# Kernel tuning notes

Hardware: AMD Instinct MI355X
Metric: run time of the kernel (lower is better)

The kernel has to match this reference:

```python
import jax, jax.numpy as jnp
import numpy as np

NUM_HEADS = 8
D_CONV = 4
NORMALIZER = 16.0
LN_EPS = 1e-5


def setup_inputs() -> dict:
    key = jax.random.key(0)
    ks = jax.random.split(key, 9)
    B, L, E = 4, 2048, 1024
    dk = E // 2
    return {
        "x": jax.random.normal(ks[0], (B, L, E), jnp.float32),
        "conv_w": jax.random.normal(ks[1], (E, D_CONV), jnp.float32) * 0.3,
        "wq": jax.random.normal(ks[2], (E, dk), jnp.float32) * 0.02,
        "wkg": jax.random.normal(ks[3], (E, dk), jnp.float32) * 0.02,
        "wv": jax.random.normal(ks[4], (E, E), jnp.float32) * 0.02,
        "wg": jax.random.normal(ks[5], (E, E), jnp.float32) * 0.02,
        "bg": jax.random.normal(ks[6], (E,), jnp.float32) * 0.02,
        "wout": jax.random.normal(ks[7], (E, E), jnp.float32) * 0.02,
        "aug_balance": jax.random.normal(ks[8], (dk,), jnp.float32) * 0.1,
    }


def _causal_dwconv_silu(x, w):
    # x: [B, L, E]; w: [E, W] depthwise kernel. Causal: left-pad W-1 zeros.
    xt = jnp.transpose(x, (0, 2, 1))  # [B, E, L]
    y = jax.lax.conv_general_dilated(
        xt, w[:, None, :], window_strides=(1,), padding=[(w.shape[1] - 1, 0)],
        feature_group_count=x.shape[-1], dimension_numbers=("NCH", "OIH", "NCH"))
    return jnp.transpose(jax.nn.silu(y), (0, 2, 1))  # [B, L, E]


def _gla(q, k, v, gk, scale):
    # Gated linear attention recurrence (fused_chunk_gla math):
    #   S_t = S_{t-1} * exp(gk_t)[:, None] + k_t (outer) v_t
    #   o_t = (scale * q_t) @ S_t
    # q, k, gk: [B,H,L,Dk]; v: [B,H,L,Dv]
    B, H, L, Dk = q.shape
    Dv = v.shape[-1]

    def step(S, inp):
        qt, kt, vt, gt = inp  # [B,H,Dk], [B,H,Dk], [B,H,Dv], [B,H,Dk]
        S = S * jnp.exp(gt)[..., None] + kt[..., None] * vt[..., None, :]
        ot = jnp.einsum("bhk,bhkv->bhv", qt * scale, S)
        return S, ot

    mv = lambda a: jnp.moveaxis(a, 2, 0)  # L to leading axis for scan
    S0 = jnp.zeros((B, H, Dk, Dv), q.dtype)
    _, o = jax.lax.scan(step, S0, (mv(q), mv(k), mv(v), mv(gk)))
    return jnp.moveaxis(o, 0, 2)  # [B,H,L,Dv]


def reference(x, conv_w, wq, wkg, wv, wg, bg, wout, aug_balance):
    B, L, E = x.shape
    H = NUM_HEADS
    xc = _causal_dwconv_silu(x, conv_w)
    q = xc @ wq            # [B,L,dk]
    kg = xc @ wkg          # [B,L,dk]
    v = xc @ wv            # [B,L,E]
    g = xc @ wg + bg       # [B,L,E]

    gk = jax.nn.log_sigmoid(kg) / NORMALIZER
    k = 1.0 - jnp.exp(gk)

    dkh = q.shape[-1] // H  # key_dim per head
    to_heads = lambda t: t.reshape(B, L, H, -1).transpose(0, 2, 1, 3)
    qh, kh, vh, gkh = to_heads(q), to_heads(k), to_heads(v), to_heads(gk)

    scale = dkh ** -0.5
    o = _gla(qh, kh, vh, gkh, scale)  # [B,H,L,head_dim]

    # Augmented term: aug_w[b,h,l] = sum_d q[b,h,l,d] * aug[h,d] * k[b,h,l,d]
    aug = aug_balance.reshape(H, dkh)
    aug_w = jnp.einsum("bhld,hd,bhld->bhl", qh, aug, kh)
    o = o + jax.nn.sigmoid(aug_w[..., None] * vh)

    # LayerNorm over head_dim, no affine
    mu = o.mean(-1, keepdims=True)
    var = o.var(-1, keepdims=True)
    o = (o - mu) * jax.lax.rsqrt(var + LN_EPS)

    o = o.transpose(0, 2, 1, 3).reshape(B, L, E)
    return (jax.nn.silu(g) * o) @ wout
```

## Files before the change

kernel.cpp:

```cpp
#include <hip/hip_runtime.h>
#include <stdint.h>

typedef unsigned short u16;
typedef unsigned int u32;
typedef __attribute__((ext_vector_type(4))) float f32x4;
typedef __attribute__((ext_vector_type(8))) short short8;
typedef __attribute__((ext_vector_type(8))) _Float16 f16x8;

#define H 8
#define LSEQ 2048
#define E 1024
#define DK 512
#define DVH 128
#define DKH 64
#define NCHUNK 32
#define MROWS 8192
#define LN_EPS 1e-5f

static __device__ __forceinline__ float bf2f(u16 u) {
    union { float f; u32 i; } v; v.i = ((u32)u) << 16; return v.f;
}
static __device__ __forceinline__ u16 f2bf(float f) {
    union { float f; u32 i; } v; v.f = f;
    u32 r = v.i + 0x7FFFu + ((v.i >> 16) & 1u);
    return (u16)(r >> 16);
}

__global__ __launch_bounds__(256) void k_conv(const float* __restrict__ x,
                                              const float* __restrict__ cw,
                                              u16* __restrict__ xc) {
    const int l0 = blockIdx.x * 64;
    const int c  = blockIdx.y * 256 + threadIdx.x;
    const int b  = blockIdx.z;
    const f32x4 w = *(const f32x4*)(cw + c * 4);
    const float* base = x + (size_t)b * LSEQ * E + c;
    u16* ob = xc + (size_t)b * LSEQ * E + c;
    float x3 = (l0 >= 3) ? base[(size_t)(l0 - 3) * E] : 0.f;
    float x2 = (l0 >= 2) ? base[(size_t)(l0 - 2) * E] : 0.f;
    float x1 = (l0 >= 1) ? base[(size_t)(l0 - 1) * E] : 0.f;
#pragma unroll 8
    for (int r = 0; r < 64; r++) {
        const float x0 = base[(size_t)(l0 + r) * E];
        float a = x3 * w[0];
        a = fmaf(x2, w[1], a);
        a = fmaf(x1, w[2], a);
        a = fmaf(x0, w[3], a);
        const float s = a / (1.f + __expf(-a));
        ob[(size_t)(l0 + r) * E] = f2bf(s);
        x3 = x2; x2 = x1; x1 = x0;
    }
}

__global__ __launch_bounds__(256) void k_transpose_all(const float* __restrict__ wq,
                                                       const float* __restrict__ wkg,
                                                       const float* __restrict__ wv,
                                                       const float* __restrict__ wg,
                                                       const float* __restrict__ wout,
                                                       u16* __restrict__ wcat,
                                                       u16* __restrict__ woutT) {
    __shared__ float tile[32][33];
    const int z = blockIdx.z;
    const float* src; u16* dst; int Ncols;
    if (z == 0)      { src = wq;   dst = wcat;                        Ncols = 512; }
    else if (z == 1) { src = wkg;  dst = wcat + (size_t)512 * 1024;   Ncols = 512; }
    else if (z == 2) { src = wv;   dst = wcat + (size_t)1024 * 1024;  Ncols = 1024; }
    else if (z == 3) { src = wg;   dst = wcat + (size_t)2048 * 1024;  Ncols = 1024; }
    else             { src = wout; dst = woutT;                       Ncols = 1024; }
    const int n0 = blockIdx.x * 32, k0 = blockIdx.y * 32;
    if (n0 >= Ncols) return;
    const int K = 1024;
    const int tx = threadIdx.x & 31, ty = threadIdx.x >> 5;
#pragma unroll
    for (int p = 0; p < 4; p++) {
        const int r = p * 8 + ty;
        tile[r][tx] = src[(size_t)(k0 + r) * Ncols + n0 + tx];
    }
    __syncthreads();
#pragma unroll
    for (int p = 0; p < 4; p++) {
        const int rn = p * 8 + ty;
        dst[(size_t)(n0 + rn) * K + k0 + tx] = f2bf(tile[tx][rn]);
    }
}

template <int MODE>
__global__ __launch_bounds__(512, 1) void k_gemm(const u16* __restrict__ A,
                                                 const u16* __restrict__ Bt,
                                                 const int N, const int K,
                                                 u16* __restrict__ oQ, u16* __restrict__ oKG,
                                                 u16* __restrict__ oV, u16* __restrict__ oSG,
                                                 const float* __restrict__ bg,
                                                 float* __restrict__ oF) {
    __shared__ __align__(16) u16 smem[4][12288];
    const int tid = threadIdx.x;
    const int lane = tid & 63, wv = tid >> 6;
    const int wm = wv >> 1, wn = wv & 1;

    const int id = blockIdx.y * gridDim.x + blockIdx.x;
    const int bx = ((id & 7) << 2) | ((id >> 3) & 3);
    const int by = id >> 5;

    const size_t rowBase = (size_t)bx * 256;
    const size_t colBase = (size_t)by * 128;

    auto stageA = [&](int hh) {
        u16* slotA = &smem[hh & 3][0];
        const u16* g = A + rowBase * K + hh * 32;
#pragma unroll
        for (int i = 0; i < 2; i++) {
            const int r = i * 128 + wv * 16 + (lane >> 2);
            const int sg = (lane & 3) ^ ((r >> 1) & 3);
            __builtin_amdgcn_global_load_lds(
                (const __attribute__((address_space(1))) void*)(g + (size_t)r * K + sg * 8),
                (__attribute__((address_space(3))) void*)(slotA + i * 4096 + wv * 512), 16, 0, 0);
        }
    };
    auto stageB = [&](int hh) {
        u16* slotB = &smem[hh & 3][8192];
        const u16* g = Bt + colBase * K + hh * 32;
        const int r = wv * 16 + (lane >> 2);
        const int sg = (lane & 3) ^ ((r >> 1) & 3);
        __builtin_amdgcn_global_load_lds(
            (const __attribute__((address_space(1))) void*)(g + (size_t)r * K + sg * 8),
            (__attribute__((address_space(3))) void*)(slotB + wv * 512), 16, 0, 0);
    };

    f32x4 acc[4][4];
#pragma unroll
    for (int m = 0; m < 4; m++)
#pragma unroll
        for (int n = 0; n < 4; n++) acc[m][n] = (f32x4){0.f, 0.f, 0.f, 0.f};

    const int rsub = lane & 15;
    const int cgl = lane >> 4;

    stageA(0); stageB(0);
    stageA(1); stageB(1);
    stageA(2); stageB(2);

    const int NT2 = K >> 5;
    for (int h = 0; h < NT2; h++) {
        const int rem = NT2 - 1 - h;
        if (rem >= 2)      asm volatile("s_waitcnt vmcnt(6)" ::: "memory");
        else if (rem == 1) asm volatile("s_waitcnt vmcnt(3)" ::: "memory");
        else               asm volatile("s_waitcnt vmcnt(0)" ::: "memory");
        asm volatile("s_barrier" ::: "memory");
        const u16* As = &smem[h & 3][0];
        const u16* Bs = As + 8192;
        short8 af[4], bfr[4];
#pragma unroll
        for (int mi = 0; mi < 4; mi++) {
            const int row = wm * 64 + mi * 16 + rsub;
            const int g = cgl ^ ((row >> 1) & 3);
            af[mi] = *(const short8*)(As + row * 32 + g * 8);
        }
#pragma unroll
        for (int ni = 0; ni < 4; ni++) {
            const int row = wn * 64 + ni * 16 + rsub;
            const int g = cgl ^ ((row >> 1) & 3);
            bfr[ni] = *(const short8*)(Bs + row * 32 + g * 8);
        }
        if (h + 3 < NT2) { stageA(h + 3); stageB(h + 3); }
        asm volatile("s_waitcnt lgkmcnt(0)" ::: "memory");
        __builtin_amdgcn_s_setprio(1);
#pragma unroll
        for (int mi = 0; mi < 4; mi++)
#pragma unroll
            for (int ni = 0; ni < 4; ni++)
                acc[mi][ni] = __builtin_amdgcn_mfma_f32_16x16x32_bf16(af[mi], bfr[ni], acc[mi][ni], 0, 0, 0);
        __builtin_amdgcn_s_setprio(0);
    }

    const int r0 = (lane >> 4) * 4;
    if (MODE == 0) {
        u16* lds = &smem[0][0];
        const bool isSG = (colBase >= 2048);
        float bgv[4];
        if (isSG) {
#pragma unroll
            for (int ni = 0; ni < 4; ni++)
                bgv[ni] = bg[colBase - 2048 + wn * 64 + ni * 16 + rsub];
        }
        asm volatile("s_barrier" ::: "memory");
#pragma unroll
        for (int mi = 0; mi < 4; mi++)
#pragma unroll
            for (int ni = 0; ni < 4; ni++) {
                const int lcol = wn * 64 + ni * 16 + rsub;
#pragma unroll
                for (int r = 0; r < 4; r++) {
                    const int lrow = wm * 64 + mi * 16 + r0 + r;
                    float val = acc[mi][ni][r];
                    if (isSG) { const float y = val + bgv[ni]; val = y / (1.f + __expf(-y)); }
                    lds[lrow * 128 + lcol] = f2bf(val);
                }
            }
        asm volatile("s_barrier" ::: "memory");
        u16* seg; int stride; size_t c0;
        if (colBase < 512)       { seg = oQ;  stride = 512;  c0 = colBase; }
        else if (colBase < 1024) { seg = oKG; stride = 512;  c0 = colBase - 512; }
        else if (colBase < 2048) { seg = oV;  stride = 1024; c0 = colBase - 1024; }
        else                     { seg = oSG; stride = 1024; c0 = colBase - 2048; }
#pragma unroll
        for (int i = 0; i < 8; i++) {
            const int unit = i * 512 + tid;
            const int row = unit >> 4, u = unit & 15;
            const uint4 vv = *(const uint4*)(lds + row * 128 + u * 8);
            *(uint4*)(seg + (rowBase + row) * stride + c0 + u * 8) = vv;
        }
    } else {
#pragma unroll
        for (int mi = 0; mi < 4; mi++)
#pragma unroll
            for (int ni = 0; ni < 4; ni++) {
                const size_t col = colBase + wn * 64 + ni * 16 + rsub;
#pragma unroll
                for (int r = 0; r < 4; r++) {
                    const size_t row = rowBase + wm * 64 + mi * 16 + r0 + r;
                    oF[row * (size_t)N + col] = acc[mi][ni][r];
                }
            }
    }
}

__global__ __launch_bounds__(256) void k_gla1(const u16* __restrict__ q,
                                              const u16* __restrict__ kg,
                                              const u16* __restrict__ v,
                                              const float* __restrict__ aug,
                                              u16* __restrict__ qt,
                                              u16* __restrict__ obuf,
                                              float* __restrict__ Sd,
                                              float* __restrict__ Dc,
                                              float* __restrict__ augw) {
    __shared__ __align__(16) float    s_f[64][68];
    __shared__ __align__(16) _Float16 s_q[64][72];
    __shared__ __align__(16) _Float16 s_k[64][72];
    __shared__ __align__(16) _Float16 s_kT[64][72];
    __shared__ __align__(16) _Float16 s_a[64][72];
    __shared__ __align__(16) _Float16 s_vT[128][72];
    const int c = blockIdx.x, bh = blockIdx.y;
    const int b = bh >> 3, h = bh & 7;
    const int tid = threadIdx.x;
    const size_t rowBase = (size_t)b * LSEQ + c * 64;
    const size_t sdBase = (size_t)bh * NCHUNK + c;

    const int tA = tid >> 2, g4 = tid & 3;
    uint4 qr0, qr1;
    {
        const int d0 = g4 * 16;
        const u16* kp = kg + (rowBase + tA) * DK + h * 64 + d0;
        const uint4 k0 = *(const uint4*)kp;
        const uint4 k1 = *(const uint4*)(kp + 8);
        const u16 kv[16] = {
            (u16)(k0.x & 0xffff), (u16)(k0.x >> 16), (u16)(k0.y & 0xffff), (u16)(k0.y >> 16),
            (u16)(k0.z & 0xffff), (u16)(k0.z >> 16), (u16)(k0.w & 0xffff), (u16)(k0.w >> 16),
            (u16)(k1.x & 0xffff), (u16)(k1.x >> 16), (u16)(k1.y & 0xffff), (u16)(k1.y >> 16),
            (u16)(k1.z & 0xffff), (u16)(k1.z >> 16), (u16)(k1.w & 0xffff), (u16)(k1.w >> 16) };
#pragma unroll
        for (int j = 0; j < 16; j++) {
            const float xk = bf2f(kv[j]);
            const float ls = fminf(xk, 0.f) - __logf(1.f + __expf(-fabsf(xk)));
            s_f[tA][d0 + j] = ls * (1.f / 16.f);
        }
        const u16* qp = q + (rowBase + tA) * DK + h * 64 + d0;
        qr0 = *(const uint4*)qp;
        qr1 = *(const uint4*)(qp + 8);

        const int dv0 = g4 * 32;
        const u16* vp = v + (rowBase + tA) * E + h * 128 + dv0;
#pragma unroll
        for (int j8 = 0; j8 < 32; j8 += 8) {
            const uint4 u = *(const uint4*)(vp + j8);
            s_vT[dv0 + j8 + 0][tA] = (_Float16)bf2f((u16)(u.x & 0xffff));
            s_vT[dv0 + j8 + 1][tA] = (_Float16)bf2f((u16)(u.x >> 16));
            s_vT[dv0 + j8 + 2][tA] = (_Float16)bf2f((u16)(u.y & 0xffff));
            s_vT[dv0 + j8 + 3][tA] = (_Float16)bf2f((u16)(u.y >> 16));
            s_vT[dv0 + j8 + 4][tA] = (_Float16)bf2f((u16)(u.z & 0xffff));
            s_vT[dv0 + j8 + 5][tA] = (_Float16)bf2f((u16)(u.z >> 16));
            s_vT[dv0 + j8 + 6][tA] = (_Float16)bf2f((u16)(u.w & 0xffff));
            s_vT[dv0 + j8 + 7][tA] = (_Float16)bf2f((u16)(u.w >> 16));
        }
    }
    __syncthreads();

    {
        const int d = tid >> 2, qseg = tid & 3;
        float part = 0.f;
#pragma unroll
        for (int j = 0; j < 16; j++) part += s_f[qseg * 16 + j][d];
        float incl = part;
        const float u1 = __shfl_up(incl, 1, 4); if (qseg >= 1) incl += u1;
        const float u2 = __shfl_up(incl, 2, 4); if (qseg >= 2) incl += u2;
        float run = incl - part;
#pragma unroll
        for (int j = 0; j < 16; j++) {
            const int t = qseg * 16 + j;
            const float g = s_f[t][d];
            run += g;
            const float kk = 1.f - __expf(g);
            const float ktil = kk * __expf(-run);
            s_k[t][d] = (_Float16)ktil;
            s_kT[d][t] = (_Float16)ktil;
            s_a[t][d] = (_Float16)kk;
            s_f[t][d] = run;
        }
    }
    __syncthreads();

    {
        const int t = tA, d0 = g4 * 16;
        const u16 qv16[16] = {
            (u16)(qr0.x & 0xffff), (u16)(qr0.x >> 16), (u16)(qr0.y & 0xffff), (u16)(qr0.y >> 16),
            (u16)(qr0.z & 0xffff), (u16)(qr0.z >> 16), (u16)(qr0.w & 0xffff), (u16)(qr0.w >> 16),
            (u16)(qr1.x & 0xffff), (u16)(qr1.x >> 16), (u16)(qr1.y & 0xffff), (u16)(qr1.y >> 16),
            (u16)(qr1.z & 0xffff), (u16)(qr1.z >> 16), (u16)(qr1.w & 0xffff), (u16)(qr1.w >> 16) };
        float qv[16];
        float augp = 0.f;
#pragma unroll
        for (int j = 0; j < 16; j++) {
            const int d = d0 + j;
            const float qraw = bf2f(qv16[j]);
            const float L = s_f[t][d];
            const float kk = (float)s_a[t][d];
            const float qtv = qraw * __expf(L) * 0.125f;
            s_q[t][d] = (_Float16)qtv;
            qv[j] = qtv;
            augp = fmaf(qraw * aug[h * 64 + d], kk, augp);
        }
        u16* qto = qt + (rowBase + t) * DK + h * 64 + d0;
#pragma unroll
        for (int j8 = 0; j8 < 16; j8 += 8) {
            uint4 u;
            u.x = (u32)f2bf(qv[j8 + 0]) | ((u32)f2bf(qv[j8 + 1]) << 16);
            u.y = (u32)f2bf(qv[j8 + 2]) | ((u32)f2bf(qv[j8 + 3]) << 16);
            u.z = (u32)f2bf(qv[j8 + 4]) | ((u32)f2bf(qv[j8 + 5]) << 16);
            u.w = (u32)f2bf(qv[j8 + 6]) | ((u32)f2bf(qv[j8 + 7]) << 16);
            *(uint4*)(qto + j8) = u;
        }
        augp += __shfl_xor(augp, 1);
        augp += __shfl_xor(augp, 2);
        if ((tid & 3) == 0) augw[(size_t)bh * LSEQ + c * 64 + t] = augp;
    }
    __syncthreads();

    const int wv = tid >> 6, lane = tid & 63;
    const int rsub = lane & 15, kq8 = (lane >> 4) * 8, r0 = (lane >> 4) * 4;
    {
#pragma unroll
        for (int si = 0; si < 4; si++) {
            if (si <= wv) {
                f32x4 acc = (f32x4){0.f, 0.f, 0.f, 0.f};
#pragma unroll
                for (int kk = 0; kk < 2; kk++) {
                    const f16x8 af = *(const f16x8*)&s_q[wv * 16 + rsub][kk * 32 + kq8];
                    const f16x8 bf = *(const f16x8*)&s_k[si * 16 + rsub][kk * 32 + kq8];
                    acc = __builtin_amdgcn_mfma_f32_16x16x32_f16(af, bf, acc, 0, 0, 0);
                }
                const int scol = si * 16 + rsub;
#pragma unroll
                for (int r = 0; r < 4; r++) {
                    const int trow = wv * 16 + r0 + r;
                    const float val = (scol <= trow) ? acc[r] : 0.f;
                    s_a[trow][scol] = (_Float16)val;
                }
            } else {
#pragma unroll
                for (int r = 0; r < 4; r++)
                    s_a[wv * 16 + r0 + r][si * 16 + rsub] = (_Float16)0.f;
            }
        }
    }
    __syncthreads();

    {
        f32x4 oacc[8];
#pragma unroll
        for (int n = 0; n < 8; n++) oacc[n] = (f32x4){0.f, 0.f, 0.f, 0.f};
        const f16x8 a0 = *(const f16x8*)&s_a[wv * 16 + rsub][kq8];
        const f16x8 a1 = *(const f16x8*)&s_a[wv * 16 + rsub][32 + kq8];
#pragma unroll
        for (int n = 0; n < 8; n++) {
            const f16x8 b0 = *(const f16x8*)&s_vT[n * 16 + rsub][kq8];
            const f16x8 b1 = *(const f16x8*)&s_vT[n * 16 + rsub][32 + kq8];
            oacc[n] = __builtin_amdgcn_mfma_f32_16x16x32_f16(a0, b0, oacc[n], 0, 0, 0);
            oacc[n] = __builtin_amdgcn_mfma_f32_16x16x32_f16(a1, b1, oacc[n], 0, 0, 0);
        }
        u16* ob = obuf + ((size_t)bh * LSEQ + c * 64) * DVH;
#pragma unroll
        for (int n = 0; n < 8; n++) {
            const int dv = n * 16 + rsub;
#pragma unroll
            for (int r = 0; r < 4; r++) {
                const int trow = wv * 16 + r0 + r;
                ob[(size_t)trow * DVH + dv] = f2bf(oacc[n][r]);
            }
        }
    }

    {
        f32x4 sacc[8];
#pragma unroll
        for (int n = 0; n < 8; n++) sacc[n] = (f32x4){0.f, 0.f, 0.f, 0.f};
        const f16x8 a0 = *(const f16x8*)&s_kT[wv * 16 + rsub][kq8];
        const f16x8 a1 = *(const f16x8*)&s_kT[wv * 16 + rsub][32 + kq8];
#pragma unroll
        for (int n = 0; n < 8; n++) {
            const f16x8 b0 = *(const f16x8*)&s_vT[n * 16 + rsub][kq8];
            const f16x8 b1 = *(const f16x8*)&s_vT[n * 16 + rsub][32 + kq8];
            sacc[n] = __builtin_amdgcn_mfma_f32_16x16x32_f16(a0, b0, sacc[n], 0, 0, 0);
            sacc[n] = __builtin_amdgcn_mfma_f32_16x16x32_f16(a1, b1, sacc[n], 0, 0, 0);
        }
        float dend[4];
#pragma unroll
        for (int r = 0; r < 4; r++) dend[r] = __expf(s_f[63][wv * 16 + r0 + r]);
#pragma unroll
        for (int n = 0; n < 8; n++) {
            const int dv = n * 16 + rsub;
#pragma unroll
            for (int r = 0; r < 4; r++) {
                const int d = wv * 16 + r0 + r;
                Sd[(sdBase * DKH + d) * DVH + dv] = sacc[n][r] * dend[r];
            }
        }
        if (rsub == 0) {
#pragma unroll
            for (int r = 0; r < 4; r++) {
                const int d = wv * 16 + r0 + r;
                Dc[sdBase * DKH + d] = dend[r];
            }
        }
    }
}

__global__ __launch_bounds__(256) void k_gla2(float* __restrict__ Sd,
                                              const float* __restrict__ Dc) {
    const int cid = blockIdx.x * 256 + threadIdx.x;
    const int bh = cid >> 13;
    const int e = cid & 8191;
    const int d = e >> 7;
    float run = 0.f;
    const size_t base = (size_t)bh * NCHUNK * 8192 + e;
    for (int c = 0; c < NCHUNK; c++) {
        const size_t idx = base + (size_t)c * 8192;
        const float dl = Sd[idx];
        Sd[idx] = run;
        run = fmaf(Dc[((size_t)bh * NCHUNK + c) * DKH + d], run, dl);
    }
}

__global__ __launch_bounds__(256) void k_gla3(const u16* __restrict__ qt,
                                              const u16* __restrict__ v,
                                              const u16* __restrict__ sg,
                                              const u16* __restrict__ obuf,
                                              const float* __restrict__ Ss,
                                              const float* __restrict__ augw,
                                              u16* __restrict__ a2) {
    __shared__ __align__(16) float s_S[64][132];
    __shared__ __align__(16) float s_qtT[64][68];
    const int c = blockIdx.x, bh = blockIdx.y;
    const int b = bh >> 3, h = bh & 7;
    const int tid = threadIdx.x;
    const size_t rowBase = (size_t)b * LSEQ + c * 64;
    {
        const int d = tid >> 2, dv0 = (tid & 3) * 32;
        const float* sp = Ss + (((size_t)bh * NCHUNK + c) * DKH + d) * DVH + dv0;
#pragma unroll
        for (int j = 0; j < 32; j += 4) *(f32x4*)&s_S[d][dv0 + j] = *(const f32x4*)(sp + j);
    }
    {
        const int t = tid >> 2, d0 = (tid & 3) * 16;
        const u16* qp = qt + (rowBase + t) * DK + h * 64 + d0;
#pragma unroll
        for (int j = 0; j < 16; j++) s_qtT[d0 + j][t] = bf2f(qp[j]);
    }
    __syncthreads();
    const int t = tid >> 2, dv0 = (tid & 3) * 32;
    float o[32];
    const u16* op = obuf + ((size_t)bh * LSEQ + c * 64 + t) * DVH + dv0;
#pragma unroll
    for (int j8 = 0; j8 < 32; j8 += 8) {
        const uint4 u = *(const uint4*)(op + j8);
        o[j8 + 0] = bf2f((u16)(u.x & 0xffff)); o[j8 + 1] = bf2f((u16)(u.x >> 16));
        o[j8 + 2] = bf2f((u16)(u.y & 0xffff)); o[j8 + 3] = bf2f((u16)(u.y >> 16));
        o[j8 + 4] = bf2f((u16)(u.z & 0xffff)); o[j8 + 5] = bf2f((u16)(u.z >> 16));
        o[j8 + 6] = bf2f((u16)(u.w & 0xffff)); o[j8 + 7] = bf2f((u16)(u.w >> 16));
    }
    for (int d = 0; d < 64; d++) {
        const float qv = s_qtT[d][t];
        const float* srow = &s_S[d][dv0];
#pragma unroll
        for (int j = 0; j < 32; j += 4) {
            const f32x4 sv = *(const f32x4*)(srow + j);
            o[j + 0] = fmaf(qv, sv[0], o[j + 0]);
            o[j + 1] = fmaf(qv, sv[1], o[j + 1]);
            o[j + 2] = fmaf(qv, sv[2], o[j + 2]);
            o[j + 3] = fmaf(qv, sv[3], o[j + 3]);
        }
    }
    const float aw = augw[(size_t)bh * LSEQ + c * 64 + t];
    const u16* vp = v + (rowBase + t) * E + h * 128 + dv0;
#pragma unroll
    for (int j8 = 0; j8 < 32; j8 += 8) {
        const uint4 u = *(const uint4*)(vp + j8);
        const float vv[8] = {
            bf2f((u16)(u.x & 0xffff)), bf2f((u16)(u.x >> 16)),
            bf2f((u16)(u.y & 0xffff)), bf2f((u16)(u.y >> 16)),
            bf2f((u16)(u.z & 0xffff)), bf2f((u16)(u.z >> 16)),
            bf2f((u16)(u.w & 0xffff)), bf2f((u16)(u.w >> 16)) };
#pragma unroll
        for (int j = 0; j < 8; j++)
            o[j8 + j] += 1.f / (1.f + __expf(-aw * vv[j]));
    }
    float sum = 0.f;
#pragma unroll
    for (int j = 0; j < 32; j++) sum += o[j];
    sum += __shfl_xor(sum, 1); sum += __shfl_xor(sum, 2);
    const float mu = sum * (1.f / 128.f);
    float sq = 0.f;
#pragma unroll
    for (int j = 0; j < 32; j++) { const float dlt = o[j] - mu; sq = fmaf(dlt, dlt, sq); }
    sq += __shfl_xor(sq, 1); sq += __shfl_xor(sq, 2);
    const float rs = rsqrtf(sq * (1.f / 128.f) + LN_EPS);
    const u16* sp2 = sg + (rowBase + t) * E + h * 128 + dv0;
    u16* ap = a2 + (rowBase + t) * E + h * 128 + dv0;
#pragma unroll
    for (int j8 = 0; j8 < 32; j8 += 8) {
        const uint4 us = *(const uint4*)(sp2 + j8);
        const float sv[8] = {
            bf2f((u16)(us.x & 0xffff)), bf2f((u16)(us.x >> 16)),
            bf2f((u16)(us.y & 0xffff)), bf2f((u16)(us.y >> 16)),
            bf2f((u16)(us.z & 0xffff)), bf2f((u16)(us.z >> 16)),
            bf2f((u16)(us.w & 0xffff)), bf2f((u16)(us.w >> 16)) };
        uint4 u;
        u.x = (u32)f2bf(sv[0] * ((o[j8 + 0] - mu) * rs)) | ((u32)f2bf(sv[1] * ((o[j8 + 1] - mu) * rs)) << 16);
        u.y = (u32)f2bf(sv[2] * ((o[j8 + 2] - mu) * rs)) | ((u32)f2bf(sv[3] * ((o[j8 + 3] - mu) * rs)) << 16);
        u.z = (u32)f2bf(sv[4] * ((o[j8 + 4] - mu) * rs)) | ((u32)f2bf(sv[5] * ((o[j8 + 5] - mu) * rs)) << 16);
        u.w = (u32)f2bf(sv[6] * ((o[j8 + 6] - mu) * rs)) | ((u32)f2bf(sv[7] * ((o[j8 + 7] - mu) * rs)) << 16);
        *(uint4*)(ap + j8) = u;
    }
}

extern "C" void kernel_launch(void* const* d_in, const int* in_sizes, int n_in,
                              void* d_out, int out_size, void* d_ws, size_t ws_size,
                              hipStream_t stream) {
    const float* x      = (const float*)d_in[0];
    const float* conv_w = (const float*)d_in[1];
    const float* wq     = (const float*)d_in[2];
    const float* wkg    = (const float*)d_in[3];
    const float* wv     = (const float*)d_in[4];
    const float* wg     = (const float*)d_in[5];
    const float* bg     = (const float*)d_in[6];
    const float* wout   = (const float*)d_in[7];
    const float* aug    = (const float*)d_in[8];

    char* ws = (char*)d_ws;
    size_t off = 0;
    auto alloc = [&](size_t bytes) -> char* {
        char* p = ws + off;
        off += (bytes + 255) & ~(size_t)255;
        return p;
    };
    u16* xc    = (u16*)alloc((size_t)MROWS * E * 2);
    u16* wcat  = (u16*)alloc((size_t)3072 * E * 2);
    u16* woutT = (u16*)alloc((size_t)E * E * 2);
    u16* qb    = (u16*)alloc((size_t)MROWS * DK * 2);
    u16* kgb   = (u16*)alloc((size_t)MROWS * DK * 2);
    u16* vb    = (u16*)alloc((size_t)MROWS * E * 2);
    u16* sgb   = (u16*)alloc((size_t)MROWS * E * 2);
    u16* qtb   = (u16*)alloc((size_t)MROWS * DK * 2);
    u16* obuf  = (u16*)alloc((size_t)32 * LSEQ * DVH * 2);
    float* Dc  = (float*)alloc((size_t)32 * NCHUNK * DKH * 4);
    float* augw= (float*)alloc((size_t)32 * LSEQ * 4);
    u16* a2    = qb;
    float* Sd  = (float*)d_out;

    k_conv<<<dim3(LSEQ / 64, E / 256, 4), 256, 0, stream>>>(x, conv_w, xc);
    k_transpose_all<<<dim3(32, 32, 5), 256, 0, stream>>>(wq, wkg, wv, wg, wout, wcat, woutT);
    k_gemm<0><<<dim3(MROWS / 256, 3072 / 128), 512, 0, stream>>>(xc, wcat, 3072, 1024,
                                                                 qb, kgb, vb, sgb, bg, nullptr);
    k_gla1<<<dim3(NCHUNK, 32), 256, 0, stream>>>(qb, kgb, vb, aug, qtb, obuf, Sd, Dc, augw);
    k_gla2<<<1024, 256, 0, stream>>>(Sd, Dc);
    k_gla3<<<dim3(NCHUNK, 32), 256, 0, stream>>>(qtb, vb, sgb, obuf, Sd, augw, a2);
    k_gemm<1><<<dim3(MROWS / 256, 1024 / 128), 512, 0, stream>>>(a2, woutT, 1024, 1024,
                                                                 nullptr, nullptr, nullptr, nullptr,
                                                                 nullptr, (float*)d_out);
}
```

Before: 189.1 us.

## Retile projection GEMM to 128x384 tiles and store chunk states in bf16

The fused QKV/gate projection GEMM now has its own kernel. Each block computes a 128x384 tile with a 2x4 wave layout, on a 512-block 1D grid with a grouped swizzle, and loads operands with direct global-to-LDS loads. The epilogue writes bias plus SiLU through a wider LDS staging row. The inter-chunk prefix kernel now writes the scanned states as bf16 into a separate buffer, which halves the traffic k_gla3 reads, at some precision cost in the carried state. The output GEMM is split out as a non-templated kernel.

```diff
diff --git a/kernel.cpp b/kernel.cpp
--- a/kernel.cpp
+++ b/kernel.cpp
@@ -83,14 +83,137 @@
     }
 }
 
-template <int MODE>
-__global__ __launch_bounds__(512, 1) void k_gemm(const u16* __restrict__ A,
-                                                 const u16* __restrict__ Bt,
-                                                 const int N, const int K,
-                                                 u16* __restrict__ oQ, u16* __restrict__ oKG,
-                                                 u16* __restrict__ oV, u16* __restrict__ oSG,
-                                                 const float* __restrict__ bg,
-                                                 float* __restrict__ oF) {
+__global__ __launch_bounds__(512, 1) void k_gemm0(const u16* __restrict__ A,
+                                                  const u16* __restrict__ Bt,
+                                                  u16* __restrict__ oQ, u16* __restrict__ oKG,
+                                                  u16* __restrict__ oV, u16* __restrict__ oSG,
+                                                  const float* __restrict__ bg) {
+    const int K = 1024;
+    __shared__ __align__(16) u16 smem[4][16384];
+    const int tid = threadIdx.x;
+    const int lane = tid & 63, wv = tid >> 6;
+    const int wm = wv >> 2, wn = wv & 3;
+
+    const int id = blockIdx.x;
+    const int local = id >> 3;
+    const int bx = ((id & 7) << 3) | (local & 7);
+    const int by = local >> 3;
+
+    const size_t rowBase = (size_t)bx * 128;
+    const size_t colBase = (size_t)by * 384;
+
+    const int rowIn = lane >> 2;
+    const int uIn = lane & 3;
+
+    auto stageA = [&](int hh) {
+        u16* slotA = &smem[hh & 3][0];
+        const u16* g = A + rowBase * K + hh * 32;
+        const int row = wv * 16 + rowIn;
+        const int sg = uIn ^ ((row >> 1) & 3);
+        __builtin_amdgcn_global_load_lds(
+            (const __attribute__((address_space(1))) void*)(g + (size_t)row * K + sg * 8),
+            (__attribute__((address_space(3))) void*)(slotA + wv * 512), 16, 0, 0);
+    };
+    auto stageB = [&](int hh) {
+        u16* slotB = &smem[hh & 3][4096];
+        const u16* g = Bt + colBase * K + hh * 32;
+#pragma unroll
+        for (int i = 0; i < 3; i++) {
+            const int row = i * 128 + wv * 16 + rowIn;
+            const int sg = uIn ^ ((row >> 1) & 3);
+            __builtin_amdgcn_global_load_lds(
+                (const __attribute__((address_space(1))) void*)(g + (size_t)row * K + sg * 8),
+                (__attribute__((address_space(3))) void*)(slotB + i * 4096 + wv * 512), 16, 0, 0);
+        }
+    };
+
+    f32x4 acc[4][6];
+#pragma unroll
+    for (int m = 0; m < 4; m++)
+#pragma unroll
+        for (int n = 0; n < 6; n++) acc[m][n] = (f32x4){0.f, 0.f, 0.f, 0.f};
+
+    const int rsub = lane & 15;
+    const int cgl = lane >> 4;
+
+    stageA(0); stageB(0);
+    stageA(1); stageB(1);
+    stageA(2); stageB(2);
+
+    const int NT2 = K >> 5;
+    for (int h = 0; h < NT2; h++) {
+        const int rem = NT2 - 1 - h;
+        if (rem >= 2)      asm volatile("s_waitcnt vmcnt(8)" ::: "memory");
+        else if (rem == 1) asm volatile("s_waitcnt vmcnt(4)" ::: "memory");
+        else               asm volatile("s_waitcnt vmcnt(0)" ::: "memory");
+        asm volatile("s_barrier" ::: "memory");
+        const u16* As = &smem[h & 3][0];
+        const u16* Bs = As + 4096;
+        short8 af[4], bfr[6];
+#pragma unroll
+        for (int mi = 0; mi < 4; mi++) {
+            const int row = wm * 64 + mi * 16 + rsub;
+            const int g = cgl ^ ((row >> 1) & 3);
+            af[mi] = *(const short8*)(As + row * 32 + g * 8);
+        }
+#pragma unroll
+        for (int ni = 0; ni < 6; ni++) {
+            const int row = wn * 96 + ni * 16 + rsub;
+            const int g = cgl ^ ((row >> 1) & 3);
+            bfr[ni] = *(const short8*)(Bs + row * 32 + g * 8);
+        }
+        if (h + 3 < NT2) { stageA(h + 3); stageB(h + 3); }
+        asm volatile("s_waitcnt lgkmcnt(0)" ::: "memory");
+        __builtin_amdgcn_s_setprio(1);
+#pragma unroll
+        for (int mi = 0; mi < 4; mi++)
+#pragma unroll
+            for (int ni = 0; ni < 6; ni++)
+                acc[mi][ni] = __builtin_amdgcn_mfma_f32_16x16x32_bf16(af[mi], bfr[ni], acc[mi][ni], 0, 0, 0);
+        __builtin_amdgcn_s_setprio(0);
+    }
+
+    const int r0 = (lane >> 4) * 4;
+    u16* lds = &smem[0][0];
+    __syncthreads();
+#pragma unroll
+    for (int ni = 0; ni < 6; ni++) {
+        const int colg = (int)colBase + wn * 96 + ni * 16 + rsub;
+        const bool isSG = (colg >= 2048);
+        const float bgv = isSG ? bg[colg - 2048] : 0.f;
+#pragma unroll
+        for (int mi = 0; mi < 4; mi++) {
+            const int lcol = wn * 96 + ni * 16 + rsub;
+#pragma unroll
+            for (int r = 0; r < 4; r++) {
+                const int lrow = wm * 64 + mi * 16 + r0 + r;
+                float val = acc[mi][ni][r];
+                if (isSG) { const float y = val + bgv; val = y / (1.f + __expf(-y)); }
+                lds[lrow * 384 + lcol] = f2bf(val);
+            }
+        }
+    }
+    __syncthreads();
+    if (lane < 48) {
+        const int col = (int)colBase + lane * 8;
+        u16* seg; int stride; int c0;
+        if (col < 512)       { seg = oQ;  stride = 512;  c0 = col; }
+        else if (col < 1024) { seg = oKG; stride = 512;  c0 = col - 512; }
+        else if (col < 2048) { seg = oV;  stride = 1024; c0 = col - 1024; }
+        else                 { seg = oSG; stride = 1024; c0 = col - 2048; }
+#pragma unroll
+        for (int rr = 0; rr < 16; rr++) {
+            const int lrow = wv * 16 + rr;
+            const uint4 vv = *(const uint4*)(lds + lrow * 384 + lane * 8);
+            *(uint4*)(seg + (rowBase + lrow) * (size_t)stride + c0) = vv;
+        }
+    }
+}
+
+__global__ __launch_bounds__(512, 1) void k_gemm1(const u16* __restrict__ A,
+                                                  const u16* __restrict__ Bt,
+                                                  float* __restrict__ oF) {
+    const int K = 1024, N = 1024;
     __shared__ __align__(16) u16 smem[4][12288];
     const int tid = threadIdx.x;
     const int lane = tid & 63, wv = tid >> 6;
@@ -172,55 +295,17 @@
     }
 
     const int r0 = (lane >> 4) * 4;
-    if (MODE == 0) {
-        u16* lds = &smem[0][0];
-        const bool isSG = (colBase >= 2048);
-        float bgv[4];
-        if (isSG) {
-#pragma unroll
-            for (int ni = 0; ni < 4; ni++)
-                bgv[ni] = bg[colBase - 2048 + wn * 64 + ni * 16 + rsub];
-        }
-        asm volatile("s_barrier" ::: "memory");
-#pragma unroll
-        for (int mi = 0; mi < 4; mi++)
-#pragma unroll
-            for (int ni = 0; ni < 4; ni++) {
-                const int lcol = wn * 64 + ni * 16 + rsub;
-#pragma unroll
-                for (int r = 0; r < 4; r++) {
-                    const int lrow = wm * 64 + mi * 16 + r0 + r;
-                    float val = acc[mi][ni][r];
-                    if (isSG) { const float y = val + bgv[ni]; val = y / (1.f + __expf(-y)); }
-                    lds[lrow * 128 + lcol] = f2bf(val);
-                }
+#pragma unroll
+    for (int mi = 0; mi < 4; mi++)
+#pragma unroll
+        for (int ni = 0; ni < 4; ni++) {
+            const size_t col = colBase + wn * 64 + ni * 16 + rsub;
+#pragma unroll
+            for (int r = 0; r < 4; r++) {
+                const size_t row = rowBase + wm * 64 + mi * 16 + r0 + r;
+                oF[row * (size_t)N + col] = acc[mi][ni][r];
             }
-        asm volatile("s_barrier" ::: "memory");
-        u16* seg; int stride; size_t c0;
-        if (colBase < 512)       { seg = oQ;  stride = 512;  c0 = colBase; }
-        else if (colBase < 1024) { seg = oKG; stride = 512;  c0 = colBase - 512; }
-        else if (colBase < 2048) { seg = oV;  stride = 1024; c0 = colBase - 1024; }
-        else                     { seg = oSG; stride = 1024; c0 = colBase - 2048; }
-#pragma unroll
-        for (int i = 0; i < 8; i++) {
-            const int unit = i * 512 + tid;
-            const int row = unit >> 4, u = unit & 15;
-            const uint4 vv = *(const uint4*)(lds + row * 128 + u * 8);
-            *(uint4*)(seg + (rowBase + row) * stride + c0 + u * 8) = vv;
-        }
-    } else {
-#pragma unroll
-        for (int mi = 0; mi < 4; mi++)
-#pragma unroll
-            for (int ni = 0; ni < 4; ni++) {
-                const size_t col = colBase + wn * 64 + ni * 16 + rsub;
-#pragma unroll
-                for (int r = 0; r < 4; r++) {
-                    const size_t row = rowBase + wm * 64 + mi * 16 + r0 + r;
-                    oF[row * (size_t)N + col] = acc[mi][ni][r];
-                }
-            }
-    }
+        }
 }
 
 __global__ __launch_bounds__(256) void k_gla1(const u16* __restrict__ q,
@@ -432,7 +517,8 @@
     }
 }
 
-__global__ __launch_bounds__(256) void k_gla2(float* __restrict__ Sd,
+__global__ __launch_bounds__(256) void k_gla2(const float* __restrict__ Sd,
+                                              u16* __restrict__ Ss,
                                               const float* __restrict__ Dc) {
     const int cid = blockIdx.x * 256 + threadIdx.x;
     const int bh = cid >> 13;
@@ -443,7 +529,7 @@
     for (int c = 0; c < NCHUNK; c++) {
         const size_t idx = base + (size_t)c * 8192;
         const float dl = Sd[idx];
-        Sd[idx] = run;
+        Ss[idx] = f2bf(run);
         run = fmaf(Dc[((size_t)bh * NCHUNK + c) * DKH + d], run, dl);
     }
 }
@@ -452,7 +538,7 @@
                                               const u16* __restrict__ v,
                                               const u16* __restrict__ sg,
                                               const u16* __restrict__ obuf,
-                                              const float* __restrict__ Ss,
+                                              const u16* __restrict__ Ss,
                                               const float* __restrict__ augw,
                                               u16* __restrict__ a2) {
     __shared__ __align__(16) float s_S[64][132];
@@ -463,9 +549,19 @@
     const size_t rowBase = (size_t)b * LSEQ + c * 64;
     {
         const int d = tid >> 2, dv0 = (tid & 3) * 32;
-        const float* sp = Ss + (((size_t)bh * NCHUNK + c) * DKH + d) * DVH + dv0;
-#pragma unroll
-        for (int j = 0; j < 32; j += 4) *(f32x4*)&s_S[d][dv0 + j] = *(const f32x4*)(sp + j);
+        const u16* sp = Ss + (((size_t)bh * NCHUNK + c) * DKH + d) * DVH + dv0;
+#pragma unroll
+        for (int j8 = 0; j8 < 32; j8 += 8) {
+            const uint4 u = *(const uint4*)(sp + j8);
+            s_S[d][dv0 + j8 + 0] = bf2f((u16)(u.x & 0xffff));
+            s_S[d][dv0 + j8 + 1] = bf2f((u16)(u.x >> 16));
+            s_S[d][dv0 + j8 + 2] = bf2f((u16)(u.y & 0xffff));
+            s_S[d][dv0 + j8 + 3] = bf2f((u16)(u.y >> 16));
+            s_S[d][dv0 + j8 + 4] = bf2f((u16)(u.z & 0xffff));
+            s_S[d][dv0 + j8 + 5] = bf2f((u16)(u.z >> 16));
+            s_S[d][dv0 + j8 + 6] = bf2f((u16)(u.w & 0xffff));
+            s_S[d][dv0 + j8 + 7] = bf2f((u16)(u.w >> 16));
+        }
     }
     {
         const int t = tid >> 2, d0 = (tid & 3) * 16;
@@ -569,6 +665,7 @@
     u16* sgb   = (u16*)alloc((size_t)MROWS * E * 2);
     u16* qtb   = (u16*)alloc((size_t)MROWS * DK * 2);
     u16* obuf  = (u16*)alloc((size_t)32 * LSEQ * DVH * 2);
+    u16* Ssb   = (u16*)alloc((size_t)32 * NCHUNK * DKH * DVH * 2);
     float* Dc  = (float*)alloc((size_t)32 * NCHUNK * DKH * 4);
     float* augw= (float*)alloc((size_t)32 * LSEQ * 4);
     u16* a2    = qb;
@@ -576,12 +673,9 @@
 
     k_conv<<<dim3(LSEQ / 64, E / 256, 4), 256, 0, stream>>>(x, conv_w, xc);
     k_transpose_all<<<dim3(32, 32, 5), 256, 0, stream>>>(wq, wkg, wv, wg, wout, wcat, woutT);
-    k_gemm<0><<<dim3(MROWS / 256, 3072 / 128), 512, 0, stream>>>(xc, wcat, 3072, 1024,
-                                                                 qb, kgb, vb, sgb, bg, nullptr);
+    k_gemm0<<<512, 512, 0, stream>>>(xc, wcat, qb, kgb, vb, sgb, bg);
     k_gla1<<<dim3(NCHUNK, 32), 256, 0, stream>>>(qb, kgb, vb, aug, qtb, obuf, Sd, Dc, augw);
-    k_gla2<<<1024, 256, 0, stream>>>(Sd, Dc);
-    k_gla3<<<dim3(NCHUNK, 32), 256, 0, stream>>>(qtb, vb, sgb, obuf, Sd, augw, a2);
-    k_gemm<1><<<dim3(MROWS / 256, 1024 / 128), 512, 0, stream>>>(a2, woutT, 1024, 1024,
-                                                                 nullptr, nullptr, nullptr, nullptr,
-                                                                 nullptr, (float*)d_out);
-}
+    k_gla2<<<1024, 256, 0, stream>>>(Sd, Ssb, Dc);
+    k_gla3<<<dim3(NCHUNK, 32), 256, 0, stream>>>(qtb, vb, sgb, obuf, Ssb, augw, a2);
+    k_gemm1<<<dim3(32, 8), 512, 0, stream>>>(a2, woutT, (float*)d_out);
+}
```

New measurement: 198.6 us. 5.1% more time.
